# Performance work log

Hardware: AMD Instinct MI355X
Metric: run time of the kernel (lower is better)

Reference implementation:

```python
import jax, jax.numpy as jnp
import numpy as np

T = 64          # frames
N = 256         # pole pairs -> Np = 2N+1 = 513
JOINTS = 512
BATCH = 32
N_ITER = 30
LAMBDA = 0.1
TOL = 1e-5


def setup_inputs() -> dict:
    key = jax.random.key(0)
    k1, k2, k3 = jax.random.split(key, 3)
    y = jax.random.normal(k1, (BATCH, T, JOINTS), dtype=jnp.float32)
    # poles near the unit circle: radius in [0.85, 1.15], angles in [0, 2*pi)
    r = 0.85 + 0.3 * jax.random.uniform(k2, (N,), dtype=jnp.float32)
    theta = 2.0 * jnp.pi * jax.random.uniform(k3, (N,), dtype=jnp.float32)
    return {"y": y, "r": r, "theta": theta}


def _soft_threshold(x, tau):
    return jnp.sign(x) * jnp.maximum(jnp.abs(x) - tau, 0.0)


def _build_dictionary(r, theta, t_len):
    # rows i = 0..T-1: [1, r^i * cos(i*theta), r^i * sin(i*theta)]  -> [T, 2N+1]
    i = jnp.arange(t_len, dtype=r.dtype)[:, None]        # [T, 1]
    rp = r[None, :] ** i                                  # [T, N]
    ang = i * theta[None, :]                              # [T, N]
    ones = jnp.ones((t_len, 1), dtype=r.dtype)
    D_raw = jnp.concatenate([ones, rp * jnp.cos(ang), rp * jnp.sin(ang)], axis=1)  # [T, Np]
    return D_raw


def _fista(DtD, DtY, lam, n_iter, tol):
    # DtD: [Np, Np], DtY: [B, Np, J]
    L = 1.0 / jnp.linalg.norm(DtD)  # Frobenius norm, matches torch.norm
    thresh = L * lam
    B, Np, J = DtY.shape
    C0 = jnp.zeros((B, Np, J), dtype=DtY.dtype)

    def step(carry, _):
        C_prev, C_curr, t_prev, done = carry
        grad = jnp.einsum('pq,bqj->bpj', DtD, C_prev) - DtY
        C_next = _soft_threshold(C_prev - L * grad, thresh)
        conv = jnp.linalg.norm(C_next - C_curr) < tol
        frozen = done | conv  # torch breaks BEFORE applying the update
        t_next = (1.0 + jnp.sqrt(1.0 + 4.0 * t_prev ** 2)) / 2.0
        t_const = (t_prev - 1.0) / t_next
        C_prev_new = C_next + t_const * (C_next - C_curr)
        C_prev_out = jnp.where(frozen, C_prev, C_prev_new)
        C_curr_out = jnp.where(frozen, C_curr, C_next)
        t_out = jnp.where(frozen, t_prev, t_next)
        return (C_prev_out, C_curr_out, t_out, frozen), None

    init = (C0, C0, jnp.asarray(1.0, DtY.dtype), jnp.asarray(False))
    (_, C_final, _, _), _ = jax.lax.scan(step, init, None, length=n_iter)
    return C_final


def reference(y, r, theta):
    D_raw = _build_dictionary(r, theta, y.shape[1])                       # [T, Np]
    D = D_raw / jnp.linalg.norm(D_raw, axis=0, keepdims=True)             # normalize_dict=True
    DtD = D.T @ D                                                          # [Np, Np]
    DtY = jnp.einsum('tp,btj->bpj', D, y)                                  # [B, Np, J]
    C_pred = _fista(DtD, DtY, LAMBDA, N_ITER, TOL)                         # [B, Np, J]
    # reconstruction uses the UN-normalized dictionary (self.dictionary_)
    Y_pred = jnp.einsum('tp,bpj->btj', D_raw, C_pred)                      # [B, T, J]
    return (Y_pred, C_pred)
```

## Files before the change

### kernel.cpp

```cpp
#include <hip/hip_runtime.h>
#include <hip/hip_bf16.h>
#include <cmath>

#define NP    513
#define NPP   516
#define T_LEN 64
#define JNT   512
#define NITER 30

#define DTD_STR  544
#define DTD_F    (640 * DTD_STR)
#define LN_OFF   DTD_F
#define Y_ELEMS  1048576

#define O_DRAWT 0
#define O_D     32832
#define O_DTY   65856
#define O_DG1H  8978752
#define O_DG1L  8996160
#define O_DTGH  9013568
#define O_DTGL  9032000

#define MPAD  576
#define PSTR  544
#define LDSTR 552
#define USTRU 72
#define LTSTR 548
#define LDSJ  16
#define LDS_BYTES (2 * LDSJ * LDSTR * 2 + 2 * LDSJ * USTRU * 2 + LDSJ * LTSTR * 4)

typedef short short8 __attribute__((ext_vector_type(8)));
typedef float f32x4  __attribute__((ext_vector_type(4)));

__device__ __forceinline__ unsigned short f2bf(float f) {
    unsigned u = __float_as_uint(f);
    return (unsigned short)((u + 0x7fffu + ((u >> 16) & 1u)) >> 16);
}
__device__ __forceinline__ float bf2f(unsigned short h) {
    return __uint_as_float((unsigned)h << 16);
}
__device__ __forceinline__ void split2(float f, unsigned short& h, unsigned short& l) {
    unsigned short hs = f2bf(f);
    h = hs;
    l = f2bf(f - bf2f(hs));
}
__device__ __forceinline__ unsigned short f2bf_cvt(float f) {
    union { __hip_bfloat16 b; unsigned short u; } cv;
    cv.b = __float2bfloat16(f);
    return cv.u;
}
__device__ __forceinline__ void split2_cvt(float f, unsigned short& h, unsigned short& l) {
    unsigned short hs = f2bf_cvt(f);
    h = hs;
    l = f2bf_cvt(f - bf2f(hs));
}

__global__ void build_D(const float* __restrict__ r, const float* __restrict__ th,
                        float* __restrict__ ws) {
    int p = blockIdx.x;
    int t = threadIdx.x;
    float val;
    if (p == 0) {
        val = 1.0f;
    } else if (p <= 256) {
        int n = p - 1;
        val = powf(r[n], (float)t) * cosf((float)t * th[n]);
    } else {
        int n = p - 257;
        val = powf(r[n], (float)t) * sinf((float)t * th[n]);
    }
    float s = val * val;
    #pragma unroll
    for (int off = 32; off; off >>= 1) s += __shfl_xor(s, off);
    float norm = sqrtf(s);
    ws[O_DRAWT + p * 64 + t] = val;
    ws[O_D + t * NPP + p]    = val / norm;
}

__global__ void dtd_kernel(const float* __restrict__ ws, float* __restrict__ dtd_out) {
    int idx = blockIdx.x * 256 + threadIdx.x;
    if (idx >= NP * NP) return;
    int p = idx / NP, q = idx % NP;
    const float* D = ws + O_D;
    float s = 0.0f;
    #pragma unroll 8
    for (int t = 0; t < T_LEN; t++) s = fmaf(D[t * NPP + p], D[t * NPP + q], s);
    dtd_out[(size_t)p * DTD_STR + q] = s;
}

__global__ __launch_bounds__(256) void lnorm1(const float* __restrict__ dtd_s,
                                              float* __restrict__ ln) {
    __shared__ float sm[256];
    int tid = threadIdx.x;
    size_t base = (size_t)blockIdx.x * 5440;
    float acc = 0.0f;
    for (int i = tid; i < 1360; i += 256) {
        float4 v = *(const float4*)&dtd_s[base + (size_t)i * 4];
        acc += v.x * v.x + v.y * v.y + v.z * v.z + v.w * v.w;
    }
    sm[tid] = acc; __syncthreads();
    for (int off = 128; off; off >>= 1) {
        if (tid < off) sm[tid] += sm[tid + off];
        __syncthreads();
    }
    if (tid == 0) ln[blockIdx.x] = sm[0];
}

__global__ void lnorm2(float* __restrict__ ln) {
    int lane = threadIdx.x;
    float v = ln[lane];
    #pragma unroll
    for (int off = 32; off; off >>= 1) v += __shfl_xor(v, off);
    if (lane == 0) {
        float L = 1.0f / sqrtf(v);
        ln[64] = L;
        ln[65] = L * 0.1f;
    }
}

__global__ void build_dg1(const float* __restrict__ ws,
                          unsigned short* __restrict__ Dg1h,
                          unsigned short* __restrict__ Dg1l) {
    int idx = blockIdx.x * 256 + threadIdx.x;
    if (idx >= 68 * 64 * 8) return;
    int i = idx & 7, t = (idx >> 3) & 63, kc8 = idx >> 9;
    int q = kc8 * 8 + i;
    float v = (q < NPP) ? ws[O_D + t * NPP + q] : 0.0f;
    unsigned short h, l;
    split2(v, h, l);
    Dg1h[idx] = h;
    Dg1l[idx] = l;
}

__global__ void build_dtg(const float* __restrict__ ws,
                          unsigned short* __restrict__ Dtgh,
                          unsigned short* __restrict__ Dtgl) {
    int idx = blockIdx.x * 256 + threadIdx.x;
    if (idx >= 8 * 576 * 8) return;
    int i = idx & 7, p = (idx >> 3) % 576, tc = idx / 4608;
    int t = tc * 8 + i;
    float v = (p < NP) ? ws[O_D + t * NPP + p] : 0.0f;
    unsigned short h, l;
    split2(v, h, l);
    Dtgh[idx] = h;
    Dtgl[idx] = l;
}

__global__ __launch_bounds__(256) void dty_kernel(const float* __restrict__ y,
                                                  const float* __restrict__ ws,
                                                  const float* __restrict__ lnv,
                                                  float* __restrict__ ldty) {
    __shared__ float As[T_LEN][64];
    __shared__ float Bs[T_LEN][64];
    int tid = threadIdx.x;
    int p0 = blockIdx.x * 64, j0 = blockIdx.y * 64, b = blockIdx.z;
    const float* D = ws + O_D;
    #pragma unroll
    for (int i = 0; i < 4; i++) {
        int lin = i * 256 + tid;
        int kt = lin >> 4, pg = lin & 15;
        float4 v = make_float4(0, 0, 0, 0);
        int pp = p0 + pg * 4;
        if (pp < NPP) v = *(const float4*)&D[kt * NPP + pp];
        *(float4*)&As[kt][pg * 4] = v;
    }
    #pragma unroll
    for (int i = 0; i < 4; i++) {
        int lin = i * 256 + tid;
        int kt = lin >> 4, jg = lin & 15;
        *(float4*)&Bs[kt][jg * 4] =
            *(const float4*)&y[((size_t)b * T_LEN + kt) * JNT + j0 + jg * 4];
    }
    __syncthreads();
    int ty = tid >> 4, tx = tid & 15;
    float acc[4][4] = {};
    #pragma unroll 8
    for (int k = 0; k < T_LEN; k++) {
        float4 a  = *(float4*)&As[k][ty * 4];
        float4 bv = *(float4*)&Bs[k][tx * 4];
        float av[4] = {a.x, a.y, a.z, a.w};
        float bw[4] = {bv.x, bv.y, bv.z, bv.w};
        #pragma unroll
        for (int i2 = 0; i2 < 4; i2++)
            #pragma unroll
            for (int jj = 0; jj < 4; jj++)
                acc[i2][jj] = fmaf(av[i2], bw[jj], acc[i2][jj]);
    }
    float L = lnv[64];
    int p = p0 + ty * 4;
    if (p < PSTR) {
        #pragma unroll
        for (int jj = 0; jj < 4; jj++) {
            int j = j0 + tx * 4 + jj;
            float4 o = make_float4(acc[0][jj] * L, acc[1][jj] * L,
                                   acc[2][jj] * L, acc[3][jj] * L);
            *(float4*)&ldty[((size_t)b * JNT + j) * PSTR + p] = o;
        }
    }
}

__global__ __launch_bounds__(512, 4) void fista_persist(
    const unsigned short* __restrict__ Dg1h,
    const unsigned short* __restrict__ Dg1l,
    const unsigned short* __restrict__ Dtgh,
    const unsigned short* __restrict__ Dtgl,
    const float* __restrict__ ldty,
    const float* __restrict__ lnv,
    float* __restrict__ Cg)
{
    extern __shared__ unsigned short smv[];
    unsigned short* BhL = smv;
    unsigned short* BlL = smv + LDSJ * LDSTR;
    unsigned short* UhL = smv + 2 * LDSJ * LDSTR;
    unsigned short* UlL = UhL + LDSJ * USTRU;
    float* ldtyL = (float*)(UhL + 2 * LDSJ * USTRU);
    int tid = threadIdx.x;
    int jb = blockIdx.x, b = blockIdx.y;
    int lane = tid & 63, w = tid >> 6;
    int l15 = lane & 15, l4 = lane >> 4;

    {
        unsigned* p32 = (unsigned*)smv;
        for (int i = tid; i < LDSJ * LDSTR; i += 512) p32[i] = 0u;
    }
    {
        const float* src = ldty + ((size_t)b * JNT + jb * 16) * PSTR;
        for (int i = tid; i < LDSJ * 136; i += 512) {
            int row = i / 136, c4 = (i % 136) * 4;
            float4 v = *(const float4*)&src[(size_t)row * PSTR + c4];
            *(float4*)&ldtyL[row * LTSTR + c4] = v;
        }
    }

    float L = lnv[64], thr = lnv[65];

    f32x4 ccur[5];
    #pragma unroll
    for (int mi = 0; mi < 5; ++mi) ccur[mi] = (f32x4){0, 0, 0, 0};
    __syncthreads();

    float t_prev = 1.0f;

    #pragma unroll 1
    for (int it = 0; it < NITER; ++it) {
        float t_next = (1.0f + sqrtf(1.0f + 4.0f * t_prev * t_prev)) * 0.5f;
        float tc = (t_prev - 1.0f) / t_next;
        t_prev = t_next;

        if (it > 0 && w < 4) {
            int srow = l15 * LDSTR + l4 * 8;
            size_t ntoff = (size_t)(w * 16 + l15);
            f32x4 a1 = (f32x4){0, 0, 0, 0};
            short8 bhA = *(const short8*)&Dg1h[((size_t)l4 * 64 + ntoff) * 8];
            short8 blA = *(const short8*)&Dg1l[((size_t)l4 * 64 + ntoff) * 8];
            #pragma unroll 1
            for (int kc = 0; kc < 17; ++kc) {
                short8 bh = bhA, bl = blA;
                if (kc < 16) {
                    size_t bo = ((size_t)((kc + 1) * 4 + l4) * 64 + ntoff) * 8;
                    bhA = *(const short8*)&Dg1h[bo];
                    blA = *(const short8*)&Dg1l[bo];
                }
                short8 sh = *(const short8*)&BhL[srow + kc * 32];
                short8 sl = *(const short8*)&BlL[srow + kc * 32];
                a1 = __builtin_amdgcn_mfma_f32_16x16x32_bf16(sh, bh, a1, 0, 0, 0);
                a1 = __builtin_amdgcn_mfma_f32_16x16x32_bf16(sl, bh, a1, 0, 0, 0);
                a1 = __builtin_amdgcn_mfma_f32_16x16x32_bf16(sh, bl, a1, 0, 0, 0);
            }
            #pragma unroll
            for (int rr = 0; rr < 4; ++rr) {
                int j = l4 * 4 + rr;
                int t = w * 16 + l15;
                unsigned short h, l;
                split2_cvt(a1[rr], h, l);
                UhL[j * USTRU + t] = h;
                UlL[j * USTRU + t] = l;
            }
        }
        __syncthreads();

        #pragma unroll
        for (int mi = 0; mi < 5; ++mi) {
            if (mi == 4 && w != 7) continue;
            int p = w * 64 + mi * 16 + l4 * 4;
            f32x4 acc = (f32x4){0, 0, 0, 0};
            if (it > 0) {
                short8 dh[2], dl[2];
                #pragma unroll
                for (int kc2 = 0; kc2 < 2; ++kc2) {
                    size_t o = ((size_t)(kc2 * 4 + l4) * MPAD + w * 64 + mi * 16 + l15) * 8;
                    dh[kc2] = *(const short8*)&Dtgh[o];
                    dl[kc2] = *(const short8*)&Dtgl[o];
                }
                #pragma unroll
                for (int kc2 = 0; kc2 < 2; ++kc2) {
                    int uo = l15 * USTRU + kc2 * 32 + l4 * 8;
                    short8 uh = *(const short8*)&UhL[uo];
                    short8 ul = *(const short8*)&UlL[uo];
                    acc = __builtin_amdgcn_mfma_f32_16x16x32_bf16(dh[kc2], uh, acc, 0, 0, 0);
                    acc = __builtin_amdgcn_mfma_f32_16x16x32_bf16(dl[kc2], uh, acc, 0, 0, 0);
                    acc = __builtin_amdgcn_mfma_f32_16x16x32_bf16(dh[kc2], ul, acc, 0, 0, 0);
                }
            }
            if (p <= 512) {
                float4 dv = *(const float4*)&ldtyL[l15 * LTSTR + p];
                float dvv[4] = {dv.x, dv.y, dv.z, dv.w};
                int lo = l15 * LDSTR + p;
                ushort4 h4 = *(const ushort4*)&BhL[lo];
                ushort4 g4 = *(const ushort4*)&BlL[lo];
                unsigned short hh[4] = {h4.x, h4.y, h4.z, h4.w};
                unsigned short gg[4] = {g4.x, g4.y, g4.z, g4.w};
                unsigned short nh[4], nl[4];
                #pragma unroll
                for (int rr = 0; rr < 4; ++rr) {
                    float cp = bf2f(hh[rr]) + bf2f(gg[rr]);
                    float v  = cp - L * acc[rr] + dvv[rr];
                    float a  = fabsf(v) - thr;
                    float st = (a > 0.0f) ? copysignf(a, v) : 0.0f;
                    float po = st + tc * (st - ccur[mi][rr]);
                    ccur[mi][rr] = st;
                    split2_cvt(po, nh[rr], nl[rr]);
                }
                *(ushort4*)&BhL[lo] = make_ushort4(nh[0], nh[1], nh[2], nh[3]);
                *(ushort4*)&BlL[lo] = make_ushort4(nl[0], nl[1], nl[2], nl[3]);
            }
        }
        __syncthreads();
    }

    #pragma unroll
    for (int mi = 0; mi < 5; ++mi) {
        if (mi == 4 && w != 7) continue;
        int pq = w * 64 + mi * 16 + l4 * 4;
        if (pq > 512) continue;
        int j = jb * 16 + l15;
        #pragma unroll
        for (int rr = 0; rr < 4; ++rr) {
            int p = pq + rr;
            if (p < NP) Cg[((size_t)b * NP + p) * JNT + j] = ccur[mi][rr];
        }
    }
}

__global__ __launch_bounds__(256) void ypred_kernel(const float* __restrict__ ws_c,
                                                    const float* __restrict__ C,
                                                    float* __restrict__ Y) {
    __shared__ float As[32][64];
    __shared__ float Bs[32][64];
    int tid = threadIdx.x;
    int j0 = blockIdx.x * 64, b = blockIdx.y;
    const float* DrawT = ws_c + O_DRAWT;
    float acc[4][4] = {};
    int ty = tid >> 4, tx = tid & 15;
    for (int kc = 0; kc < 17; kc++) {
        int p0 = kc * 32;
        #pragma unroll
        for (int i = 0; i < 2; i++) {
            int lin = i * 256 + tid;
            int kp = lin >> 4, tg = lin & 15;
            float4 v = make_float4(0, 0, 0, 0);
            int p = p0 + kp;
            if (p < NP) v = *(const float4*)&DrawT[(size_t)p * 64 + tg * 4];
            *(float4*)&As[kp][tg * 4] = v;
        }
        #pragma unroll
        for (int i = 0; i < 2; i++) {
            int lin = i * 256 + tid;
            int kp = lin >> 4, jg = lin & 15;
            float4 v = make_float4(0, 0, 0, 0);
            int p = p0 + kp;
            if (p < NP) v = *(const float4*)&C[((size_t)b * NP + p) * JNT + j0 + jg * 4];
            *(float4*)&Bs[kp][jg * 4] = v;
        }
        __syncthreads();
        #pragma unroll
        for (int k = 0; k < 32; k++) {
            float4 a  = *(float4*)&As[k][ty * 4];
            float4 bv = *(float4*)&Bs[k][tx * 4];
            float av[4] = {a.x, a.y, a.z, a.w};
            float bw[4] = {bv.x, bv.y, bv.z, bv.w};
            #pragma unroll
            for (int i2 = 0; i2 < 4; i2++)
                #pragma unroll
                for (int jj = 0; jj < 4; jj++)
                    acc[i2][jj] = fmaf(av[i2], bw[jj], acc[i2][jj]);
        }
        __syncthreads();
    }
    #pragma unroll
    for (int i2 = 0; i2 < 4; i2++) {
        int t = ty * 4 + i2;
        size_t base = ((size_t)b * T_LEN + t) * JNT + j0 + tx * 4;
        *(float4*)&Y[base] = make_float4(acc[i2][0], acc[i2][1], acc[i2][2], acc[i2][3]);
    }
}

extern "C" void kernel_launch(void* const* d_in, const int* in_sizes, int n_in,
                              void* d_out, int out_size, void* d_ws, size_t ws_size,
                              hipStream_t stream) {
    const float* y  = (const float*)d_in[0];
    const float* r  = (const float*)d_in[1];
    const float* th = (const float*)d_in[2];
    float* ws   = (float*)d_ws;
    float* out  = (float*)d_out;
    float* dtd  = out;
    float* ln   = out + LN_OFF;
    float* Cgo  = out + Y_ELEMS;
    unsigned short* Dg1h = (unsigned short*)(ws + O_DG1H);
    unsigned short* Dg1l = (unsigned short*)(ws + O_DG1L);
    unsigned short* Dtgh = (unsigned short*)(ws + O_DTGH);
    unsigned short* Dtgl = (unsigned short*)(ws + O_DTGL);
    float* ldty  = ws + O_DTY;

    hipMemsetAsync(out,      0, (size_t)(DTD_F + 68) * 4, stream);
    hipMemsetAsync(ws + O_D, 0, (size_t)(T_LEN * NPP) * 4, stream);

    build_D<<<NP, 64, 0, stream>>>(r, th, ws);
    dtd_kernel<<<(NP * NP + 255) / 256, 256, 0, stream>>>(ws, dtd);
    lnorm1<<<64, 256, 0, stream>>>(dtd, ln);
    lnorm2<<<1, 64, 0, stream>>>(ln);
    dty_kernel<<<dim3(9, 8, 32), 256, 0, stream>>>(y, ws, ln, ldty);
    build_dg1<<<(68 * 64 * 8 + 255) / 256, 256, 0, stream>>>(ws, Dg1h, Dg1l);
    build_dtg<<<(8 * 576 * 8 + 255) / 256, 256, 0, stream>>>(ws, Dtgh, Dtgl);

    hipFuncSetAttribute((const void*)fista_persist,
                        hipFuncAttributeMaxDynamicSharedMemorySize, LDS_BYTES);
    fista_persist<<<dim3(32, 32), 512, LDS_BYTES, stream>>>(Dg1h, Dg1l, Dtgh, Dtgl,
                                                            ldty, ln, Cgo);

    ypred_kernel<<<dim3(8, 32), 256, 0, stream>>>(ws, Cgo, out);
}
```

Before: 463.2 us.

## Split first GEMM K-range across all eight waves and swizzle LDS coefficient rows

```diff
diff --git a/kernel.cpp b/kernel.cpp
--- a/kernel.cpp
+++ b/kernel.cpp
@@ -23,11 +23,11 @@
 
 #define MPAD  576
 #define PSTR  544
-#define LDSTR 552
+#define LDSTR 576
 #define USTRU 72
 #define LTSTR 548
 #define LDSJ  16
-#define LDS_BYTES (2 * LDSJ * LDSTR * 2 + 2 * LDSJ * USTRU * 2 + LDSJ * LTSTR * 4)
+#define LDS_BYTES (2 * LDSJ * LDSTR * 2 + 2 * LDSJ * USTRU * 2 + LDSJ * LTSTR * 4 + 64 * 18 * 4)
 
 typedef short short8 __attribute__((ext_vector_type(8)));
 typedef float f32x4  __attribute__((ext_vector_type(4)));
@@ -214,10 +214,12 @@
     unsigned short* UhL = smv + 2 * LDSJ * LDSTR;
     unsigned short* UlL = UhL + LDSJ * USTRU;
     float* ldtyL = (float*)(UhL + 2 * LDSJ * USTRU);
+    float* Upf   = ldtyL + LDSJ * LTSTR;
     int tid = threadIdx.x;
     int jb = blockIdx.x, b = blockIdx.y;
     int lane = tid & 63, w = tid >> 6;
     int l15 = lane & 15, l4 = lane >> 4;
+    int smaskE = (l15 & 7) << 3;
 
     {
         unsigned* p32 = (unsigned*)smv;
@@ -247,32 +249,49 @@
         float tc = (t_prev - 1.0f) / t_next;
         t_prev = t_next;
 
-        if (it > 0 && w < 4) {
-            int srow = l15 * LDSTR + l4 * 8;
-            size_t ntoff = (size_t)(w * 16 + l15);
-            f32x4 a1 = (f32x4){0, 0, 0, 0};
-            short8 bhA = *(const short8*)&Dg1h[((size_t)l4 * 64 + ntoff) * 8];
-            short8 blA = *(const short8*)&Dg1l[((size_t)l4 * 64 + ntoff) * 8];
+        int tf = w & 3, kh = w >> 2;
+        f32x4 a1 = (f32x4){0, 0, 0, 0};
+        if (it > 0) {
+            int kc0 = (kh == 0) ? 0 : 9;
+            int kc1 = (kh == 0) ? 9 : 17;
+            int srowb = l15 * LDSTR;
+            size_t ntoff = (size_t)(tf * 16 + l15);
+            int c0 = ((kc0 * 32 + l4 * 8) ^ smaskE);
+            short8 shA = *(const short8*)&BhL[srowb + c0];
+            short8 slA = *(const short8*)&BlL[srowb + c0];
+            short8 bhA = *(const short8*)&Dg1h[((size_t)(kc0 * 4 + l4) * 64 + ntoff) * 8];
+            short8 blA = *(const short8*)&Dg1l[((size_t)(kc0 * 4 + l4) * 64 + ntoff) * 8];
             #pragma unroll 1
-            for (int kc = 0; kc < 17; ++kc) {
-                short8 bh = bhA, bl = blA;
-                if (kc < 16) {
+            for (int kc = kc0; kc < kc1; ++kc) {
+                short8 sh = shA, sl = slA, bh = bhA, bl = blA;
+                if (kc + 1 < kc1) {
+                    int c = (((kc + 1) * 32 + l4 * 8) ^ smaskE);
+                    shA = *(const short8*)&BhL[srowb + c];
+                    slA = *(const short8*)&BlL[srowb + c];
                     size_t bo = ((size_t)((kc + 1) * 4 + l4) * 64 + ntoff) * 8;
                     bhA = *(const short8*)&Dg1h[bo];
                     blA = *(const short8*)&Dg1l[bo];
                 }
-                short8 sh = *(const short8*)&BhL[srow + kc * 32];
-                short8 sl = *(const short8*)&BlL[srow + kc * 32];
                 a1 = __builtin_amdgcn_mfma_f32_16x16x32_bf16(sh, bh, a1, 0, 0, 0);
                 a1 = __builtin_amdgcn_mfma_f32_16x16x32_bf16(sl, bh, a1, 0, 0, 0);
                 a1 = __builtin_amdgcn_mfma_f32_16x16x32_bf16(sh, bl, a1, 0, 0, 0);
             }
+            if (kh == 1) {
+                #pragma unroll
+                for (int rr = 0; rr < 4; ++rr)
+                    Upf[(tf * 16 + l4 * 4 + rr) * 18 + l15] = a1[rr];
+            }
+        }
+        __syncthreads();
+
+        if (it > 0 && kh == 0) {
             #pragma unroll
             for (int rr = 0; rr < 4; ++rr) {
+                float u = a1[rr] + Upf[(tf * 16 + l4 * 4 + rr) * 18 + l15];
+                unsigned short h, l;
+                split2_cvt(u, h, l);
                 int j = l4 * 4 + rr;
-                int t = w * 16 + l15;
-                unsigned short h, l;
-                split2_cvt(a1[rr], h, l);
+                int t = tf * 16 + l15;
                 UhL[j * USTRU + t] = h;
                 UlL[j * USTRU + t] = l;
             }
@@ -305,7 +324,7 @@
             if (p <= 512) {
                 float4 dv = *(const float4*)&ldtyL[l15 * LTSTR + p];
                 float dvv[4] = {dv.x, dv.y, dv.z, dv.w};
-                int lo = l15 * LDSTR + p;
+                int lo = l15 * LDSTR + (p ^ smaskE);
                 ushort4 h4 = *(const ushort4*)&BhL[lo];
                 ushort4 g4 = *(const ushort4*)&BlL[lo];
                 unsigned short hh[4] = {h4.x, h4.y, h4.z, h4.w};
```

After: 466.5 us. No clear change (+0.7%).
